# Kernel tuning notes

Measured on AMD Instinct MI355X. Metric: run time of the kernel, lower is better.

The kernel has to match this reference:

```python
import jax, jax.numpy as jnp
import numpy as np

B, N, C = 8, 4096, 768
H = 12
D = C // H            # 64
BN = C // 2           # bottleneck dim 384
EPS_LN = 1e-5
EPS_ATTN = 1e-6


def layer_norm(x, g, b):
    mu = jnp.mean(x, axis=-1, keepdims=True)
    var = jnp.mean(jnp.square(x - mu), axis=-1, keepdims=True)
    return (x - mu) * jax.lax.rsqrt(var + EPS_LN) * g + b


def setup_inputs() -> dict:
    key = jax.random.key(0)
    ks = jax.random.split(key, 8)
    s = 0.02
    return {
        "x": jax.random.normal(ks[0], (B, N, C), jnp.float32),
        "w_qkv": jax.random.normal(ks[1], (C, 3 * C), jnp.float32) * s,
        "b_qkv": jnp.zeros((3 * C,), jnp.float32),
        "w_proj": jax.random.normal(ks[2], (C, C), jnp.float32) * s,
        "b_proj": jnp.zeros((C,), jnp.float32),
        "g1": jnp.ones((C,), jnp.float32),
        "beta1": jnp.zeros((C,), jnp.float32),
        "g2": jnp.ones((C,), jnp.float32),
        "beta2": jnp.zeros((C,), jnp.float32),
        "w_down": jax.random.normal(ks[3], (C, BN), jnp.float32) * s,
        "b_down": jnp.zeros((BN,), jnp.float32),
        "w_up": jax.random.normal(ks[4], (BN, C), jnp.float32) * s,
        "b_up": jnp.zeros((C,), jnp.float32),
        "g3": jnp.ones((C,), jnp.float32),
        "beta3": jnp.zeros((C,), jnp.float32),
    }


def _linear_attention(x, w_qkv, b_qkv, w_proj, b_proj):
    # x: (B, N, C)
    qkv = x @ w_qkv + b_qkv                       # (B, N, 3C)
    qkv = qkv.reshape(B, N, 3, H, D)
    qkv = jnp.transpose(qkv, (2, 0, 3, 1, 4))     # (3, B, H, N, D)
    q, k, v = qkv[0], qkv[1], qkv[2]
    fm = lambda t: jax.nn.elu(t) + 1.0            # positive feature map
    q, k = fm(q), fm(k)
    kv = jnp.einsum('bhnd,bhnv->bhdv', k, v)      # (B, H, D, D)
    out = jnp.einsum('bhnd,bhdv->bhnv', q, kv)    # (B, H, N, D)
    k_sum = k.sum(axis=2)                         # (B, H, D)
    normalizer = jnp.einsum('bhnd,bhd->bhn', q, k_sum) + EPS_ATTN
    out = out / normalizer[..., None]
    out = jnp.transpose(out, (0, 2, 1, 3)).reshape(B, N, C)
    return out @ w_proj + b_proj


def reference(x, w_qkv, b_qkv, w_proj, b_proj, g1, beta1, g2, beta2,
              w_down, b_down, w_up, b_up, g3, beta3):
    # DinomalyBlock forward (eval mode: dropout/noise disabled)
    x = x + _linear_attention(layer_norm(x, g1, beta1), w_qkv, b_qkv, w_proj, b_proj)
    r = layer_norm(x, g2, beta2)
    h = jax.nn.gelu(r @ w_down + b_down, approximate=False)  # torch GELU default = exact
    h = h @ w_up + b_up
    return layer_norm(r + h, g3, beta3)
```

## Files before the change

kernel.cpp:

```cpp
#include <hip/hip_runtime.h>
#include <hip/hip_bf16.h>
#include <cstdio>


typedef __attribute__((ext_vector_type(8))) short short8;
typedef __attribute__((ext_vector_type(4))) float floatx4;

__device__ __forceinline__ float bf2f(unsigned short u) {
    return __uint_as_float(((unsigned int)u) << 16);
}
__device__ __forceinline__ unsigned short f2bf(float f) {
    __hip_bfloat16 h = __float2bfloat16(f);
    return *reinterpret_cast<unsigned short*>(&h);
}

__device__ __forceinline__ void async_copy16(const unsigned short* g, unsigned short* l) {
    __builtin_amdgcn_global_load_lds(
        (const __attribute__((address_space(1))) unsigned int*)g,
        (__attribute__((address_space(3))) unsigned int*)l, 16, 0, 0);
}

__global__ __launch_bounds__(256) void transpose_bf16(
    const float* __restrict__ w, unsigned short* __restrict__ wt, int K, int Nc)
{
    __shared__ float tile[32][33];
    int kb = blockIdx.x * 32, nb = blockIdx.y * 32;
    int tx = threadIdx.x, ty = threadIdx.y;
    #pragma unroll
    for (int i = 0; i < 32; i += 8)
        tile[ty + i][tx] = w[(size_t)(kb + ty + i) * Nc + nb + tx];
    __syncthreads();
    #pragma unroll
    for (int i = 0; i < 32; i += 8)
        wt[(size_t)(nb + ty + i) * K + kb + tx] = f2bf(tile[tx][ty + i]);
}

template<bool OBF16>
__global__ __launch_bounds__(256) void ln_kernel(
    const float* __restrict__ in, const float* __restrict__ gw,
    const float* __restrict__ bw, void* __restrict__ outp)
{
    int row = blockIdx.x;
    const float* x = in + (size_t)row * 768;
    int t = threadIdx.x;
    float v0 = x[t], v1 = x[t + 256], v2 = x[t + 512];
    float s = v0 + v1 + v2;
    float ss = v0 * v0 + v1 * v1 + v2 * v2;
    #pragma unroll
    for (int o = 32; o > 0; o >>= 1) {
        s += __shfl_down(s, o);
        ss += __shfl_down(ss, o);
    }
    __shared__ float red[8];
    int wave = t >> 6, lane = t & 63;
    if (lane == 0) { red[wave] = s; red[4 + wave] = ss; }
    __syncthreads();
    if (t == 0) {
        float S = red[0] + red[1] + red[2] + red[3];
        float SS = red[4] + red[5] + red[6] + red[7];
        float mu = S * (1.0f / 768.0f);
        float var = SS * (1.0f / 768.0f) - mu * mu;
        red[0] = mu;
        red[1] = rsqrtf(var + 1e-5f);
    }
    __syncthreads();
    float mu = red[0], rstd = red[1];
    #pragma unroll
    for (int e = 0; e < 3; e++) {
        int c = t + e * 256;
        float v = (e == 0) ? v0 : (e == 1) ? v1 : v2;
        float y = (v - mu) * rstd * gw[c] + bw[c];
        if (OBF16) ((unsigned short*)outp)[(size_t)row * 768 + c] = f2bf(y);
        else       ((float*)outp)[(size_t)row * 768 + c] = y;
    }
}

template<int MODE>
__global__ __launch_bounds__(256, 2) void gemm_kernel(
    const unsigned short* __restrict__ A,
    const unsigned short* __restrict__ Wt,
    const float* __restrict__ bias,
    const void* __restrict__ resv,
    void* __restrict__ outv,
    int M, int K, int Nc)
{
    __shared__ __align__(16) unsigned short As[128][32];
    __shared__ __align__(16) unsigned short Bs[128][32];
    const int row0 = blockIdx.x * 128;
    const int col0 = blockIdx.y * 128;
    const int t = threadIdx.x;
    const int lane = t & 63;
    const int wave = t >> 6;
    const int wm = (wave >> 1) * 64;
    const int wn = (wave & 1) * 64;
    const int srow = t >> 2;
    const int skc = (t & 3) * 8;
    const int frow = lane & 15;
    const int fk = (lane >> 4) * 8;

    floatx4 acc[4][4];
    #pragma unroll
    for (int i = 0; i < 4; i++)
        #pragma unroll
        for (int j = 0; j < 4; j++)
            acc[i][j] = (floatx4){0.f, 0.f, 0.f, 0.f};

    for (int k0 = 0; k0 < K; k0 += 32) {
        __syncthreads();
        async_copy16(A  + (size_t)(row0 + srow) * K + k0 + skc,       &As[wave * 16][0]);
        async_copy16(A  + (size_t)(row0 + 64 + srow) * K + k0 + skc,  &As[64 + wave * 16][0]);
        async_copy16(Wt + (size_t)(col0 + srow) * K + k0 + skc,       &Bs[wave * 16][0]);
        async_copy16(Wt + (size_t)(col0 + 64 + srow) * K + k0 + skc,  &Bs[64 + wave * 16][0]);
        __syncthreads();
        short8 af[4], bf[4];
        #pragma unroll
        for (int i = 0; i < 4; i++) af[i] = *(const short8*)&As[wm + i * 16 + frow][fk];
        #pragma unroll
        for (int j = 0; j < 4; j++) bf[j] = *(const short8*)&Bs[wn + j * 16 + frow][fk];
        #pragma unroll
        for (int i = 0; i < 4; i++)
            #pragma unroll
            for (int j = 0; j < 4; j++)
                acc[i][j] = __builtin_amdgcn_mfma_f32_16x16x32_bf16(
                    af[i], bf[j], acc[i][j], 0, 0, 0);
    }

    #pragma unroll
    for (int i = 0; i < 4; i++) {
        #pragma unroll
        for (int j = 0; j < 4; j++) {
            int col = col0 + wn + j * 16 + (lane & 15);
            float bcol = bias[col];
            #pragma unroll
            for (int rr = 0; rr < 4; rr++) {
                int row = row0 + wm + i * 16 + (lane >> 4) * 4 + rr;
                float v = acc[i][j][rr] + bcol;
                size_t idx = (size_t)row * Nc + col;
                if (MODE == 0) {
                    if (col < 1536) v = (v > 0.f) ? (v + 1.f) : expf(v);
                    ((unsigned short*)outv)[idx] = f2bf(v);
                } else if (MODE == 1) {
                    v += ((const float*)resv)[idx];
                    ((float*)outv)[idx] = v;
                } else if (MODE == 2) {
                    v = 0.5f * v * (1.0f + erff(v * 0.70710678118654752f));
                    ((unsigned short*)outv)[idx] = f2bf(v);
                } else {
                    v += bf2f(((const unsigned short*)resv)[idx]);
                    ((float*)outv)[idx] = v;
                }
            }
        }
    }
}

__global__ __launch_bounds__(256) void kv_accum(
    const unsigned short* __restrict__ qkv, float* __restrict__ kvbuf)
{
    int blk = blockIdx.x;
    int chunk = blk & 7;
    int bh = blk >> 3;
    int b = bh / 12, h = bh % 12;
    int n0 = chunk * 512;
    int t = threadIdx.x;
    int d = t & 63, g = t >> 6;
    __shared__ float kl[2][32][68];
    __shared__ float vl[2][32][68];
    float kv[16];
    #pragma unroll
    for (int j = 0; j < 16; j++) kv[j] = 0.f;
    float ks = 0.f;

    int sr = t >> 3;
    int c16 = (t & 7) * 16;
    bool isk = c16 < 64;
    int cc = isk ? c16 : c16 - 64;
    const unsigned short* gbase =
        qkv + (size_t)(b * 4096 + n0 + sr) * 2304 + (isk ? 768 : 1536) + h * 64 + cc;
    uint4 r0, r1;
    auto loadg = [&](int nb) {
        const uint4* s = (const uint4*)(gbase + (size_t)nb * 2304);
        r0 = s[0]; r1 = s[1];
    };
    auto storel = [&](int buf) {
        float* dst = isk ? &kl[buf][sr][cc] : &vl[buf][sr][cc];
        const unsigned short* u0 = (const unsigned short*)&r0;
        const unsigned short* u1 = (const unsigned short*)&r1;
        #pragma unroll
        for (int i = 0; i < 8; i++) dst[i] = bf2f(u0[i]);
        #pragma unroll
        for (int i = 0; i < 8; i++) dst[8 + i] = bf2f(u1[i]);
    };

    loadg(0);
    storel(0);
    __syncthreads();
    for (int c = 0; c < 16; c++) {
        if (c < 15) loadg((c + 1) * 32);
        int bsel = c & 1;
        #pragma unroll 8
        for (int r2 = 0; r2 < 32; r2++) {
            float kd = kl[bsel][r2][d];
            ks += kd;
            const float4* vv = (const float4*)&vl[bsel][r2][g * 16];
            float4 a0 = vv[0], a1 = vv[1], a2 = vv[2], a3 = vv[3];
            kv[0]  += kd * a0.x; kv[1]  += kd * a0.y; kv[2]  += kd * a0.z; kv[3]  += kd * a0.w;
            kv[4]  += kd * a1.x; kv[5]  += kd * a1.y; kv[6]  += kd * a1.z; kv[7]  += kd * a1.w;
            kv[8]  += kd * a2.x; kv[9]  += kd * a2.y; kv[10] += kd * a2.z; kv[11] += kd * a2.w;
            kv[12] += kd * a3.x; kv[13] += kd * a3.y; kv[14] += kd * a3.z; kv[15] += kd * a3.w;
        }
        if (c < 15) storel((c + 1) & 1);
        __syncthreads();
    }
    float* dstg = kvbuf + (size_t)bh * 4160;
    #pragma unroll
    for (int j = 0; j < 16; j++)
        atomicAdd(&dstg[(g * 16 + j) * 64 + d], kv[j]);
    if (g == 0) atomicAdd(&dstg[4096 + d], ks);
}

__global__ __launch_bounds__(256) void attn_apply(
    const unsigned short* __restrict__ qkv, const float* __restrict__ kvbuf,
    unsigned short* __restrict__ attnC)
{
    int blk = blockIdx.x;
    int nchunk = blk & 31;
    int bh = blk >> 5;
    int b = bh / 12, h = bh % 12;
    int n0 = nchunk * 128;
    int t = threadIdx.x;
    int lane = t & 63, wave = t >> 6;
    __shared__ __align__(16) unsigned short ql[128][72];
    __shared__ __align__(16) unsigned short Bs[80][72];

    {
        const float* kvg = kvbuf + (size_t)bh * 4160;
        int e = t >> 2, d0 = (t & 3) * 16;
        const float4* src4 = (const float4*)(kvg + e * 64 + d0);
        #pragma unroll
        for (int i = 0; i < 4; i++) {
            float4 v = src4[i];
            unsigned long long pk = (unsigned long long)f2bf(v.x)
                | ((unsigned long long)f2bf(v.y) << 16)
                | ((unsigned long long)f2bf(v.z) << 32)
                | ((unsigned long long)f2bf(v.w) << 48);
            *(unsigned long long*)&Bs[e][d0 + i * 4] = pk;
        }
        if (t < 64) {
            Bs[64][t] = f2bf(kvg[4096 + t]);
            #pragma unroll
            for (int r = 65; r < 80; r++) Bs[r][t] = 0;
        }
    }
    {
        int r = t >> 1, c0 = (t & 1) * 32;
        const uint4* src = (const uint4*)(qkv + (size_t)(b * 4096 + n0 + r) * 2304 + h * 64 + c0);
        uint4* dst = (uint4*)&ql[r][c0];
        #pragma unroll
        for (int i = 0; i < 4; i++) dst[i] = src[i];
    }
    __syncthreads();

    int frow = lane & 15, quad = lane >> 4;
    floatx4 acc[2][5];
    #pragma unroll
    for (int it = 0; it < 2; it++)
        #pragma unroll
        for (int jt = 0; jt < 5; jt++)
            acc[it][jt] = (floatx4){0.f, 0.f, 0.f, 0.f};

    #pragma unroll
    for (int ks = 0; ks < 2; ks++) {
        int fk = ks * 32 + quad * 8;
        short8 a0 = *(const short8*)&ql[wave * 32 + frow][fk];
        short8 a1 = *(const short8*)&ql[wave * 32 + 16 + frow][fk];
        #pragma unroll
        for (int jt = 0; jt < 5; jt++) {
            short8 bb = *(const short8*)&Bs[jt * 16 + frow][fk];
            acc[0][jt] = __builtin_amdgcn_mfma_f32_16x16x32_bf16(a0, bb, acc[0][jt], 0, 0, 0);
            acc[1][jt] = __builtin_amdgcn_mfma_f32_16x16x32_bf16(a1, bb, acc[1][jt], 0, 0, 0);
        }
    }

    #pragma unroll
    for (int it = 0; it < 2; it++) {
        #pragma unroll
        for (int rr = 0; rr < 4; rr++) {
            float nv = __shfl(acc[it][4][rr], (lane & 48));
            float inv = 1.0f / (nv + 1e-6f);
            int row = n0 + wave * 32 + it * 16 + quad * 4 + rr;
            size_t obase = (size_t)(b * 4096 + row) * 768 + h * 64;
            #pragma unroll
            for (int jt = 0; jt < 4; jt++)
                attnC[obase + jt * 16 + frow] = f2bf(acc[it][jt][rr] * inv);
        }
    }
}

extern "C" void kernel_launch(void* const* d_in, const int* in_sizes, int n_in,
                              void* d_out, int out_size, void* d_ws, size_t ws_size,
                              hipStream_t stream)
{
    const float* x      = (const float*)d_in[0];
    const float* w_qkv  = (const float*)d_in[1];
    const float* b_qkv  = (const float*)d_in[2];
    const float* w_proj = (const float*)d_in[3];
    const float* b_proj = (const float*)d_in[4];
    const float* g1     = (const float*)d_in[5];
    const float* be1    = (const float*)d_in[6];
    const float* g2     = (const float*)d_in[7];
    const float* be2    = (const float*)d_in[8];
    const float* w_down = (const float*)d_in[9];
    const float* b_down = (const float*)d_in[10];
    const float* w_up   = (const float*)d_in[11];
    const float* b_up   = (const float*)d_in[12];
    const float* g3     = (const float*)d_in[13];
    const float* be3    = (const float*)d_in[14];

    char* p = (char*)d_ws;
    auto take = [&](size_t b) { char* q = p; p += (b + 255) & ~(size_t)255; return q; };
    unsigned short* wtq  = (unsigned short*)take((size_t)2304 * 768 * 2);
    unsigned short* wtp  = (unsigned short*)take((size_t)768 * 768 * 2);
    unsigned short* wtd  = (unsigned short*)take((size_t)384 * 768 * 2);
    unsigned short* wtu  = (unsigned short*)take((size_t)768 * 384 * 2);
    unsigned short* bufA = (unsigned short*)take((size_t)32768 * 768 * 2);
    unsigned short* qkvb = (unsigned short*)take((size_t)32768 * 2304 * 2);
    float*          kvb  = (float*)take((size_t)96 * 4160 * 4);
    unsigned short* hbuf = (unsigned short*)take((size_t)32768 * 384 * 2);
    unsigned short* rbuf = qkvb;

    size_t needed = (size_t)(p - (char*)d_ws);
    if (needed > ws_size)
        fprintf(stderr, "WARNING: ws too small: need %zu have %zu\n", needed, ws_size);

    dim3 tb(32, 8);
    transpose_bf16<<<dim3(24, 72), tb, 0, stream>>>(w_qkv, wtq, 768, 2304);
    transpose_bf16<<<dim3(24, 24), tb, 0, stream>>>(w_proj, wtp, 768, 768);
    transpose_bf16<<<dim3(24, 12), tb, 0, stream>>>(w_down, wtd, 768, 384);
    transpose_bf16<<<dim3(12, 24), tb, 0, stream>>>(w_up, wtu, 384, 768);
    hipMemsetAsync(kvb, 0, (size_t)96 * 4160 * 4, stream);

    ln_kernel<true><<<32768, 256, 0, stream>>>(x, g1, be1, bufA);
    gemm_kernel<0><<<dim3(256, 18), 256, 0, stream>>>(bufA, wtq, b_qkv, nullptr, qkvb,
                                                      32768, 768, 2304);
    kv_accum<<<768, 256, 0, stream>>>(qkvb, kvb);
    attn_apply<<<3072, 256, 0, stream>>>(qkvb, kvb, bufA);
    gemm_kernel<1><<<dim3(256, 6), 256, 0, stream>>>(bufA, wtp, b_proj, x, d_out,
                                                     32768, 768, 768);
    ln_kernel<true><<<32768, 256, 0, stream>>>((const float*)d_out, g2, be2, rbuf);
    gemm_kernel<2><<<dim3(256, 3), 256, 0, stream>>>(rbuf, wtd, b_down, nullptr, hbuf,
                                                     32768, 768, 384);
    gemm_kernel<3><<<dim3(256, 6), 256, 0, stream>>>(hbuf, wtu, b_up, rbuf, d_out,
                                                     32768, 384, 768);
    ln_kernel<false><<<32768, 256, 0, stream>>>((const float*)d_out, g3, be3, (float*)d_out);
}
```

Measured before the change: 727.4 us.

## Fuse residual add into LayerNorm, widen GEMM K-tile with swizzled LDS, merge transposes

Merges the four weight-transpose launches into one kernel. The GEMM K-step grows from 32 to 64, with an XOR-swizzled LDS layout meant to avoid bank conflicts on fragment reads. GEMM epilogues now write bf16 only, and the residual add moves into new add+LayerNorm kernels, which removes the fp32 d_out round trips and halves epilogue write bytes. LayerNorm uses 384 threads with float2 loads. The trade-off is an extra bf16 intermediate buffer, bf16 rounding of the projection output before the residual add, and larger LDS use per block.

```diff
diff --git a/kernel.cpp b/kernel.cpp
--- a/kernel.cpp
+++ b/kernel.cpp
@@ -20,58 +20,124 @@
         (__attribute__((address_space(3))) unsigned int*)l, 16, 0, 0);
 }
 
-__global__ __launch_bounds__(256) void transpose_bf16(
-    const float* __restrict__ w, unsigned short* __restrict__ wt, int K, int Nc)
-{
+__global__ __launch_bounds__(256) void transpose_all(
+    const float* __restrict__ wq, const float* __restrict__ wp,
+    const float* __restrict__ wd, const float* __restrict__ wu,
+    unsigned short* __restrict__ tq, unsigned short* __restrict__ tp,
+    unsigned short* __restrict__ td, unsigned short* __restrict__ tu)
+{
+    int blk = blockIdx.x;
+    const float* w; unsigned short* o; int K, Nc, tx32;
+    if (blk < 1728)      { w = wq; o = tq; K = 768; Nc = 2304; tx32 = 24; }
+    else if (blk < 2304) { w = wp; o = tp; K = 768; Nc = 768;  tx32 = 24; blk -= 1728; }
+    else if (blk < 2592) { w = wd; o = td; K = 768; Nc = 384;  tx32 = 24; blk -= 2304; }
+    else                 { w = wu; o = tu; K = 384; Nc = 768;  tx32 = 12; blk -= 2592; }
+    int kb = (blk % tx32) * 32, nb = (blk / tx32) * 32;
     __shared__ float tile[32][33];
-    int kb = blockIdx.x * 32, nb = blockIdx.y * 32;
-    int tx = threadIdx.x, ty = threadIdx.y;
+    int tx = threadIdx.x & 31, ty = threadIdx.x >> 5;
     #pragma unroll
     for (int i = 0; i < 32; i += 8)
         tile[ty + i][tx] = w[(size_t)(kb + ty + i) * Nc + nb + tx];
     __syncthreads();
     #pragma unroll
     for (int i = 0; i < 32; i += 8)
-        wt[(size_t)(nb + ty + i) * K + kb + tx] = f2bf(tile[tx][ty + i]);
+        o[(size_t)(nb + ty + i) * K + kb + tx] = f2bf(tile[tx][ty + i]);
 }
 
 template<bool OBF16>
-__global__ __launch_bounds__(256) void ln_kernel(
+__global__ __launch_bounds__(384) void ln_kernel(
     const float* __restrict__ in, const float* __restrict__ gw,
     const float* __restrict__ bw, void* __restrict__ outp)
 {
     int row = blockIdx.x;
-    const float* x = in + (size_t)row * 768;
     int t = threadIdx.x;
-    float v0 = x[t], v1 = x[t + 256], v2 = x[t + 512];
-    float s = v0 + v1 + v2;
-    float ss = v0 * v0 + v1 * v1 + v2 * v2;
+    float2 xv = ((const float2*)(in + (size_t)row * 768))[t];
+    float s = xv.x + xv.y;
+    float ss = xv.x * xv.x + xv.y * xv.y;
     #pragma unroll
     for (int o = 32; o > 0; o >>= 1) {
         s += __shfl_down(s, o);
         ss += __shfl_down(ss, o);
     }
-    __shared__ float red[8];
+    __shared__ float red[14];
     int wave = t >> 6, lane = t & 63;
-    if (lane == 0) { red[wave] = s; red[4 + wave] = ss; }
+    if (lane == 0) { red[wave] = s; red[6 + wave] = ss; }
     __syncthreads();
     if (t == 0) {
-        float S = red[0] + red[1] + red[2] + red[3];
-        float SS = red[4] + red[5] + red[6] + red[7];
+        float S = 0.f, SS = 0.f;
+        #pragma unroll
+        for (int i = 0; i < 6; i++) { S += red[i]; SS += red[6 + i]; }
         float mu = S * (1.0f / 768.0f);
         float var = SS * (1.0f / 768.0f) - mu * mu;
-        red[0] = mu;
-        red[1] = rsqrtf(var + 1e-5f);
-    }
-    __syncthreads();
-    float mu = red[0], rstd = red[1];
-    #pragma unroll
-    for (int e = 0; e < 3; e++) {
-        int c = t + e * 256;
-        float v = (e == 0) ? v0 : (e == 1) ? v1 : v2;
-        float y = (v - mu) * rstd * gw[c] + bw[c];
-        if (OBF16) ((unsigned short*)outp)[(size_t)row * 768 + c] = f2bf(y);
-        else       ((float*)outp)[(size_t)row * 768 + c] = y;
+        red[12] = mu;
+        red[13] = rsqrtf(var + 1e-5f);
+    }
+    __syncthreads();
+    float mu = red[12], rstd = red[13];
+    float2 g = ((const float2*)gw)[t];
+    float2 b = ((const float2*)bw)[t];
+    float y0 = (xv.x - mu) * rstd * g.x + b.x;
+    float y1 = (xv.y - mu) * rstd * g.y + b.y;
+    if (OBF16) {
+        unsigned int pk = (unsigned int)f2bf(y0) | ((unsigned int)f2bf(y1) << 16);
+        ((unsigned int*)outp)[(size_t)row * 384 + t] = pk;
+    } else {
+        ((float2*)outp)[(size_t)row * 384 + t] = make_float2(y0, y1);
+    }
+}
+
+template<bool RES_F32, bool OUT_F32>
+__global__ __launch_bounds__(384) void add_ln_kernel(
+    const unsigned short* __restrict__ y, const void* __restrict__ resv,
+    const float* __restrict__ gw, const float* __restrict__ bw,
+    void* __restrict__ outp)
+{
+    int row = blockIdx.x;
+    int t = threadIdx.x;
+    unsigned int yp = ((const unsigned int*)(y + (size_t)row * 768))[t];
+    float a0 = bf2f((unsigned short)(yp & 0xffff));
+    float a1 = bf2f((unsigned short)(yp >> 16));
+    float r0, r1;
+    if (RES_F32) {
+        float2 rv = ((const float2*)((const float*)resv + (size_t)row * 768))[t];
+        r0 = rv.x; r1 = rv.y;
+    } else {
+        unsigned int rp = ((const unsigned int*)((const unsigned short*)resv + (size_t)row * 768))[t];
+        r0 = bf2f((unsigned short)(rp & 0xffff));
+        r1 = bf2f((unsigned short)(rp >> 16));
+    }
+    float v0 = a0 + r0, v1 = a1 + r1;
+    float s = v0 + v1;
+    float ss = v0 * v0 + v1 * v1;
+    #pragma unroll
+    for (int o = 32; o > 0; o >>= 1) {
+        s += __shfl_down(s, o);
+        ss += __shfl_down(ss, o);
+    }
+    __shared__ float red[14];
+    int wave = t >> 6, lane = t & 63;
+    if (lane == 0) { red[wave] = s; red[6 + wave] = ss; }
+    __syncthreads();
+    if (t == 0) {
+        float S = 0.f, SS = 0.f;
+        #pragma unroll
+        for (int i = 0; i < 6; i++) { S += red[i]; SS += red[6 + i]; }
+        float mu = S * (1.0f / 768.0f);
+        float var = SS * (1.0f / 768.0f) - mu * mu;
+        red[12] = mu;
+        red[13] = rsqrtf(var + 1e-5f);
+    }
+    __syncthreads();
+    float mu = red[12], rstd = red[13];
+    float2 g = ((const float2*)gw)[t];
+    float2 b = ((const float2*)bw)[t];
+    float y0 = (v0 - mu) * rstd * g.x + b.x;
+    float y1 = (v1 - mu) * rstd * g.y + b.y;
+    if (OUT_F32) {
+        ((float2*)outp)[(size_t)row * 384 + t] = make_float2(y0, y1);
+    } else {
+        unsigned int pk = (unsigned int)f2bf(y0) | ((unsigned int)f2bf(y1) << 16);
+        ((unsigned int*)outp)[(size_t)row * 384 + t] = pk;
     }
 }
 
@@ -80,12 +146,11 @@
     const unsigned short* __restrict__ A,
     const unsigned short* __restrict__ Wt,
     const float* __restrict__ bias,
-    const void* __restrict__ resv,
-    void* __restrict__ outv,
+    unsigned short* __restrict__ outp,
     int M, int K, int Nc)
 {
-    __shared__ __align__(16) unsigned short As[128][32];
-    __shared__ __align__(16) unsigned short Bs[128][32];
+    __shared__ __align__(16) unsigned short As[128][64];
+    __shared__ __align__(16) unsigned short Bs[128][64];
     const int row0 = blockIdx.x * 128;
     const int col0 = blockIdx.y * 128;
     const int t = threadIdx.x;
@@ -93,10 +158,10 @@
     const int wave = t >> 6;
     const int wm = (wave >> 1) * 64;
     const int wn = (wave & 1) * 64;
-    const int srow = t >> 2;
-    const int skc = (t & 3) * 8;
     const int frow = lane & 15;
-    const int fk = (lane >> 4) * 8;
+    const int quad = lane >> 4;
+    const int lrow = lane >> 3;
+    const int lchunk = (lane & 7) ^ lrow;
 
     floatx4 acc[4][4];
     #pragma unroll
@@ -105,50 +170,48 @@
         for (int j = 0; j < 4; j++)
             acc[i][j] = (floatx4){0.f, 0.f, 0.f, 0.f};
 
-    for (int k0 = 0; k0 < K; k0 += 32) {
+    for (int k0 = 0; k0 < K; k0 += 64) {
         __syncthreads();
-        async_copy16(A  + (size_t)(row0 + srow) * K + k0 + skc,       &As[wave * 16][0]);
-        async_copy16(A  + (size_t)(row0 + 64 + srow) * K + k0 + skc,  &As[64 + wave * 16][0]);
-        async_copy16(Wt + (size_t)(col0 + srow) * K + k0 + skc,       &Bs[wave * 16][0]);
-        async_copy16(Wt + (size_t)(col0 + 64 + srow) * K + k0 + skc,  &Bs[64 + wave * 16][0]);
+        #pragma unroll
+        for (int q = 0; q < 4; q++) {
+            int r = wave * 32 + q * 8 + lrow;
+            async_copy16(A  + (size_t)(row0 + r) * K + k0 + lchunk * 8, &As[wave * 32 + q * 8][0]);
+            async_copy16(Wt + (size_t)(col0 + r) * K + k0 + lchunk * 8, &Bs[wave * 32 + q * 8][0]);
+        }
         __syncthreads();
-        short8 af[4], bf[4];
-        #pragma unroll
-        for (int i = 0; i < 4; i++) af[i] = *(const short8*)&As[wm + i * 16 + frow][fk];
-        #pragma unroll
-        for (int j = 0; j < 4; j++) bf[j] = *(const short8*)&Bs[wn + j * 16 + frow][fk];
-        #pragma unroll
-        for (int i = 0; i < 4; i++)
-            #pragma unroll
-            for (int j = 0; j < 4; j++)
-                acc[i][j] = __builtin_amdgcn_mfma_f32_16x16x32_bf16(
-                    af[i], bf[j], acc[i][j], 0, 0, 0);
+        #pragma unroll
+        for (int ks = 0; ks < 2; ks++) {
+            const int pc = ((ks * 4 + quad) ^ (frow & 7)) * 8;
+            short8 af[4], bf4[4];
+            #pragma unroll
+            for (int i = 0; i < 4; i++) af[i] = *(const short8*)&As[wm + i * 16 + frow][pc];
+            #pragma unroll
+            for (int j = 0; j < 4; j++) bf4[j] = *(const short8*)&Bs[wn + j * 16 + frow][pc];
+            #pragma unroll
+            for (int i = 0; i < 4; i++)
+                #pragma unroll
+                for (int j = 0; j < 4; j++)
+                    acc[i][j] = __builtin_amdgcn_mfma_f32_16x16x32_bf16(
+                        af[i], bf4[j], acc[i][j], 0, 0, 0);
+        }
     }
 
     #pragma unroll
     for (int i = 0; i < 4; i++) {
         #pragma unroll
         for (int j = 0; j < 4; j++) {
-            int col = col0 + wn + j * 16 + (lane & 15);
+            int col = col0 + wn + j * 16 + frow;
             float bcol = bias[col];
             #pragma unroll
             for (int rr = 0; rr < 4; rr++) {
-                int row = row0 + wm + i * 16 + (lane >> 4) * 4 + rr;
+                int row = row0 + wm + i * 16 + quad * 4 + rr;
                 float v = acc[i][j][rr] + bcol;
-                size_t idx = (size_t)row * Nc + col;
                 if (MODE == 0) {
                     if (col < 1536) v = (v > 0.f) ? (v + 1.f) : expf(v);
-                    ((unsigned short*)outv)[idx] = f2bf(v);
-                } else if (MODE == 1) {
-                    v += ((const float*)resv)[idx];
-                    ((float*)outv)[idx] = v;
                 } else if (MODE == 2) {
                     v = 0.5f * v * (1.0f + erff(v * 0.70710678118654752f));
-                    ((unsigned short*)outv)[idx] = f2bf(v);
-                } else {
-                    v += bf2f(((const unsigned short*)resv)[idx]);
-                    ((float*)outv)[idx] = v;
                 }
+                outp[(size_t)row * Nc + col] = f2bf(v);
             }
         }
     }
@@ -327,30 +390,24 @@
     unsigned short* qkvb = (unsigned short*)take((size_t)32768 * 2304 * 2);
     float*          kvb  = (float*)take((size_t)96 * 4160 * 4);
     unsigned short* hbuf = (unsigned short*)take((size_t)32768 * 384 * 2);
-    unsigned short* rbuf = qkvb;
+    unsigned short* rbuf    = qkvb;
+    unsigned short* projout = qkvb + (size_t)32768 * 768;
+    unsigned short* upout   = qkvb + (size_t)2 * 32768 * 768;
 
     size_t needed = (size_t)(p - (char*)d_ws);
     if (needed > ws_size)
         fprintf(stderr, "WARNING: ws too small: need %zu have %zu\n", needed, ws_size);
 
-    dim3 tb(32, 8);
-    transpose_bf16<<<dim3(24, 72), tb, 0, stream>>>(w_qkv, wtq, 768, 2304);
-    transpose_bf16<<<dim3(24, 24), tb, 0, stream>>>(w_proj, wtp, 768, 768);
-    transpose_bf16<<<dim3(24, 12), tb, 0, stream>>>(w_down, wtd, 768, 384);
-    transpose_bf16<<<dim3(12, 24), tb, 0, stream>>>(w_up, wtu, 384, 768);
+    transpose_all<<<2880, 256, 0, stream>>>(w_qkv, w_proj, w_down, w_up, wtq, wtp, wtd, wtu);
     hipMemsetAsync(kvb, 0, (size_t)96 * 4160 * 4, stream);
 
-    ln_kernel<true><<<32768, 256, 0, stream>>>(x, g1, be1, bufA);
-    gemm_kernel<0><<<dim3(256, 18), 256, 0, stream>>>(bufA, wtq, b_qkv, nullptr, qkvb,
-                                                      32768, 768, 2304);
+    ln_kernel<true><<<32768, 384, 0, stream>>>(x, g1, be1, bufA);
+    gemm_kernel<0><<<dim3(256, 18), 256, 0, stream>>>(bufA, wtq, b_qkv, qkvb, 32768, 768, 2304);
     kv_accum<<<768, 256, 0, stream>>>(qkvb, kvb);
     attn_apply<<<3072, 256, 0, stream>>>(qkvb, kvb, bufA);
-    gemm_kernel<1><<<dim3(256, 6), 256, 0, stream>>>(bufA, wtp, b_proj, x, d_out,
-                                                     32768, 768, 768);
-    ln_kernel<true><<<32768, 256, 0, stream>>>((const float*)d_out, g2, be2, rbuf);
-    gemm_kernel<2><<<dim3(256, 3), 256, 0, stream>>>(rbuf, wtd, b_down, nullptr, hbuf,
-                                                     32768, 768, 384);
-    gemm_kernel<3><<<dim3(256, 6), 256, 0, stream>>>(hbuf, wtu, b_up, rbuf, d_out,
-                                                     32768, 384, 768);
-    ln_kernel<false><<<32768, 256, 0, stream>>>((const float*)d_out, g3, be3, (float*)d_out);
-}
+    gemm_kernel<1><<<dim3(256, 6), 256, 0, stream>>>(bufA, wtp, b_proj, projout, 32768, 768, 768);
+    add_ln_kernel<true, false><<<32768, 384, 0, stream>>>(projout, x, g2, be2, rbuf);
+    gemm_kernel<2><<<dim3(256, 3), 256, 0, stream>>>(rbuf, wtd, b_down, hbuf, 32768, 768, 384);
+    gemm_kernel<1><<<dim3(256, 6), 256, 0, stream>>>(hbuf, wtu, b_up, upout, 32768, 384, 768);
+    add_ln_kernel<false, true><<<32768, 384, 0, stream>>>(upout, rbuf, g3, be3, (float*)d_out);
+}
```

Result: faster. 698.2 us (-4.0%).
